# Performance work log

Measured on AMD Instinct MI355X. Metric: run time of the kernel, lower is better.

The kernel has to match this reference:

```python
import jax, jax.numpy as jnp
import numpy as np

B, S, D = 4, 2048, 1024
H = 3 * D  # MLP hidden


def setup_inputs() -> dict:
    key = jax.random.key(0)
    ks = jax.random.split(key, 12)
    s = 1.0 / np.sqrt(D)
    n = lambda k, shape, sc: (jax.random.normal(k, shape, jnp.float32) * sc)
    return {
        "x": n(ks[0], (B, S, D), 1.0),
        "ln1_g": jnp.ones((D,), jnp.float32), "ln1_b": jnp.zeros((D,), jnp.float32),
        "ln2_g": jnp.ones((D,), jnp.float32), "ln2_b": jnp.zeros((D,), jnp.float32),
        "Wq": n(ks[1], (D, D), s), "bq": jnp.zeros((D,), jnp.float32),
        "Wk": n(ks[2], (D, D), s), "bk": jnp.zeros((D,), jnp.float32),
        "Wv": n(ks[3], (D, D), s), "bv": jnp.zeros((D,), jnp.float32),
        "Wi": n(ks[4], (D, 1), s), "bi": jnp.zeros((1,), jnp.float32),
        "Wf": n(ks[5], (D, 1), s), "bf": jnp.zeros((1,), jnp.float32),
        "Wo": n(ks[6], (D, D), s), "bo": jnp.zeros((D,), jnp.float32),
        "W1": n(ks[7], (D, H), s), "b1": jnp.zeros((H,), jnp.float32),
        "W2": n(ks[8], (H, D), 1.0 / np.sqrt(H)), "b2": jnp.zeros((D,), jnp.float32),
    }


def _layernorm(x, g, b, eps=1e-5):
    m = jnp.mean(x, axis=-1, keepdims=True)
    v = jnp.mean(jnp.square(x - m), axis=-1, keepdims=True)
    return (x - m) * jax.lax.rsqrt(v + eps) * g + b


def reference(x, ln1_g, ln1_b, ln2_g, ln2_b, Wq, bq, Wk, bk, Wv, bv,
              Wi, bi, Wf, bf, Wo, bo, W1, b1, W2, b2):
    seq = x.shape[1]
    h = _layernorm(x, ln1_g, ln1_b)
    # q, k computed in the original but unused in the score matrix (kept faithful)
    q = h @ Wq + bq
    k = h @ Wk + bk
    v = h @ Wv + bv                                  # [B,S,D]
    log_f = jax.nn.log_sigmoid(h @ Wf + bf)          # [B,S,1]
    log_i = jax.nn.log_sigmoid(h @ Wi + bi)          # [B,S,1]
    o = jax.nn.sigmoid(h @ Wo + bo)                  # [B,S,D]
    log_f_cum = jnp.cumsum(log_f, axis=1)            # [B,S,1]
    # log_scores[b,t,s] = log_i[b,s] + log_f_cum[b,t] - log_f_cum[b,s]
    log_scores = jnp.swapaxes(log_i, 1, 2) + log_f_cum - jnp.swapaxes(log_f_cum, 1, 2)
    causal = jnp.triu(jnp.full((seq, seq), -1e9, jnp.float32), k=1)
    scores = jnp.exp(log_scores + causal[None])      # [B,S,S]
    scores = scores / (jnp.sum(scores, axis=-1, keepdims=True) + 1e-6)
    attn = scores @ v                                # [B,S,D]
    x = x + o * attn
    h2 = _layernorm(x, ln2_g, ln2_b)
    m = h2 @ W1 + b1
    m = jnp.square(jnp.where(m > 0, m, 0.01 * m))    # LeakyReLU then square
    x = x + m @ W2 + b2
    return x
```

## Files before the change

### kernel.cpp

```cpp
#include <hip/hip_runtime.h>
#include <hip/hip_bf16.h>
#include <cstdint>

#define DI __device__ __forceinline__
typedef unsigned short u16;
using f32x4 = __attribute__((ext_vector_type(4))) float;
using bf16x8 = __attribute__((ext_vector_type(8))) short;

DI float bf16_bits_to_f32(u16 h) { return __uint_as_float(((unsigned int)h) << 16); }
DI u16 f32_to_bf16_bits(float f) {
    unsigned int u = __float_as_uint(f);
    unsigned int lsb = (u >> 16) & 1u;
    u += 0x7fffu + lsb;
    return (u16)(u >> 16);
}
DI float logsigf(float z) {
    if (z >= 0.f) return -log1pf(expf(-z));
    return z - log1pf(expf(z));
}
DI float lsef(float a, float b) {
    float mx = fmaxf(a, b), mn = fminf(a, b);
    return mx + log1pf(expf(mn - mx));
}
DI void ld4(float* d, const float* s) { *(float4*)d = *(const float4*)s; }
DI bool is_bf16(const unsigned int* g1w) { return g1w[0] == 0x3F803F80u; }

struct __align__(8) U4 { u16 a, b, c, d; };
union BF8 { u16 s[8]; uint4 v; };

DI void gload_lds16(const void* gsrc, void* ldst) {
    __builtin_amdgcn_global_load_lds(
        (const __attribute__((address_space(1))) uint32_t*)gsrc,
        (__attribute__((address_space(3))) uint32_t*)ldst,
        16, 0, 0);
}

struct PrepDesc {
    const void* csrc[12];
    unsigned int cdst[12];
    int cn[12];
    const void* tsrc[4];
    unsigned int tdst[4];
    int tR[4], tCd[4];
    int tstart[5];
};
__global__ __launch_bounds__(256) void prep_kernel(
    PrepDesc pd, char* __restrict__ ws, const unsigned int* __restrict__ g1w)
{
    const bool isbf = is_bf16(g1w);
    const int bid = blockIdx.x;
    if (bid < 12) {
        const void* s = pd.csrc[bid];
        float* d = (float*)ws + pd.cdst[bid];
        const int n = pd.cn[bid];
        for (int i = threadIdx.x; i < n; i += 256)
            d[i] = isbf ? bf16_bits_to_f32(((const u16*)s)[i]) : ((const float*)s)[i];
        return;
    }
    __shared__ float tile[64][65];
    const int b2 = bid - 12;
    int e = 0;
    if (b2 >= pd.tstart[1]) e = 1;
    if (b2 >= pd.tstart[2]) e = 2;
    if (b2 >= pd.tstart[3]) e = 3;
    const int local = b2 - pd.tstart[e];
    const int R = pd.tR[e], Cd = pd.tCd[e];
    const int nbx = R >> 6;
    const int r0 = (local % nbx) * 64, c0 = (local / nbx) * 64;
    const void* src = pd.tsrc[e];
    u16* dst = (u16*)ws + pd.tdst[e];
    const int tid = threadIdx.x;
    #pragma unroll
    for (int i = 0; i < 16; ++i) {
        int idx = tid + i * 256;
        int lr = idx >> 6, lc = idx & 63;
        size_t g = (size_t)(r0 + lr) * Cd + c0 + lc;
        tile[lr][lc] = isbf ? bf16_bits_to_f32(((const u16*)src)[g]) : ((const float*)src)[g];
    }
    __syncthreads();
    #pragma unroll
    for (int i = 0; i < 16; ++i) {
        int idx = tid + i * 256;
        int lc2 = idx >> 6, lr2 = idx & 63;
        dst[(size_t)(c0 + lc2) * R + r0 + lr2] = f32_to_bf16_bits(tile[lr2][lc2]);
    }
}

DI float block_reduce_sum256(float v, float* sbuf) {
    #pragma unroll
    for (int off = 32; off > 0; off >>= 1) v += __shfl_down(v, off);
    int lane = threadIdx.x & 63, wid = threadIdx.x >> 6;
    if (lane == 0) sbuf[wid] = v;
    __syncthreads();
    float r = sbuf[0] + sbuf[1] + sbuf[2] + sbuf[3];
    __syncthreads();
    return r;
}

template<bool FI, int MODE>
__global__ __launch_bounds__(256) void ln_kernel(
    const void* __restrict__ Xv, const unsigned int* __restrict__ g1w,
    const float* __restrict__ gam, const float* __restrict__ bet,
    u16* __restrict__ Hout,
    const float* __restrict__ Wi, const float* __restrict__ bi,
    const float* __restrict__ Wf, const float* __restrict__ bf2,
    float* __restrict__ li, float* __restrict__ lf)
{
    __shared__ float sbuf[4];
    int row = blockIdx.x;
    int tid = threadIdx.x;
    size_t base = (size_t)row * 1024 + (size_t)tid * 4;
    float x[4];
    if (MODE == 2 || (MODE == 1 && is_bf16(g1w))) {
        U4 u = *(const U4*)((const u16*)Xv + base);
        x[0] = bf16_bits_to_f32(u.a); x[1] = bf16_bits_to_f32(u.b);
        x[2] = bf16_bits_to_f32(u.c); x[3] = bf16_bits_to_f32(u.d);
    } else {
        ld4(x, (const float*)Xv + base);
    }
    float s = x[0] + x[1] + x[2] + x[3];
    s = block_reduce_sum256(s, sbuf);
    float mean = s * (1.f / 1024.f);
    float d[4], ss = 0.f;
    #pragma unroll
    for (int j = 0; j < 4; ++j) { d[j] = x[j] - mean; ss += d[j] * d[j]; }
    ss = block_reduce_sum256(ss, sbuf);
    float rstd = rsqrtf(ss * (1.f / 1024.f) + 1e-5f);
    float g4[4], b4[4];
    ld4(g4, gam + tid * 4); ld4(b4, bet + tid * 4);
    float h[4];
    #pragma unroll
    for (int j = 0; j < 4; ++j) h[j] = d[j] * rstd * g4[j] + b4[j];
    U4 hu;
    hu.a = f32_to_bf16_bits(h[0]); hu.b = f32_to_bf16_bits(h[1]);
    hu.c = f32_to_bf16_bits(h[2]); hu.d = f32_to_bf16_bits(h[3]);
    *(U4*)(Hout + base) = hu;
    if (FI) {
        float wi4[4], wf4[4];
        ld4(wi4, Wi + tid * 4); ld4(wf4, Wf + tid * 4);
        float pi = 0.f, pf = 0.f;
        #pragma unroll
        for (int j = 0; j < 4; ++j) { pi += h[j] * wi4[j]; pf += h[j] * wf4[j]; }
        pi = block_reduce_sum256(pi, sbuf);
        pf = block_reduce_sum256(pf, sbuf);
        if (tid == 0) {
            li[row] = logsigf(pi + bi[0]);
            lf[row] = logsigf(pf + bf2[0]);
        }
    }
}

__global__ __launch_bounds__(1024) void gates_kernel(
    const float* __restrict__ lf, const float* __restrict__ li,
    float* __restrict__ F, float* __restrict__ rsinv, int S)
{
    __shared__ float p[1024];
    __shared__ float q[1024];
    int b = blockIdx.x, t = threadIdx.x;
    float a = lf[b * S + 2 * t], c = lf[b * S + 2 * t + 1];
    float s2 = a + c;
    p[t] = s2; __syncthreads();
    #pragma unroll
    for (int off = 1; off < 1024; off <<= 1) {
        float add = (t >= off) ? p[t - off] : 0.f;
        __syncthreads();
        p[t] += add;
        __syncthreads();
    }
    float excl = p[t] - s2;
    float F0 = excl + a, F1 = excl + s2;
    F[b * S + 2 * t] = F0; F[b * S + 2 * t + 1] = F1;
    float g0 = li[b * S + 2 * t] - F0;
    float g1 = li[b * S + 2 * t + 1] - F1;
    float m2 = lsef(g0, g1);
    q[t] = m2; __syncthreads();
    #pragma unroll
    for (int off = 1; off < 1024; off <<= 1) {
        float add = (t >= off) ? q[t - off] : -1e30f;
        __syncthreads();
        float nv = lsef(q[t], add);
        __syncthreads();
        q[t] = nv;
        __syncthreads();
    }
    float lprev = (t > 0) ? q[t - 1] : -1e30f;
    float lc0 = lsef(lprev, g0);
    float lc1 = q[t];
    rsinv[b * S + 2 * t]     = 1.f / (expf(F0 + lc0) + 1e-6f);
    rsinv[b * S + 2 * t + 1] = 1.f / (expf(F1 + lc1) + 1e-6f);
}

__global__ __launch_bounds__(256) void wgen_kernel(
    const float* __restrict__ li, const float* __restrict__ F,
    const float* __restrict__ rsinv, u16* __restrict__ Wn)
{
    const int S = 2048;
    const int i = blockIdx.y, b = blockIdx.z;
    const int t0 = i * 128;
    const int s0 = t0 - 128 + (int)blockIdx.x * 64;
    if (s0 < 0) return;
    const int tid = threadIdx.x;
    const int lane = tid & 63, wave = tid >> 6;
    const int colb = (lane & 7) * 8;
    float lv[8], fv[8];
    ld4(lv, li + b * S + s0 + colb); ld4(lv + 4, li + b * S + s0 + colb + 4);
    ld4(fv, F + b * S + s0 + colb);  ld4(fv + 4, F + b * S + s0 + colb + 4);
    float g[8];
    #pragma unroll
    for (int j = 0; j < 8; ++j) g[j] = lv[j] - fv[j];
    #pragma unroll
    for (int r = 0; r < 4; ++r) {
        int row = wave * 32 + r * 8 + (lane >> 3);
        int t = t0 + row;
        float Ft = F[b * S + t];
        float ri = rsinv[b * S + t];
        BF8 wb;
        #pragma unroll
        for (int j = 0; j < 8; ++j) {
            int sg = s0 + colb + j;
            float w = (sg <= t) ? expf(g[j] + Ft) * ri : 0.f;
            wb.s[j] = f32_to_bf16_bits(w);
        }
        *(uint4*)(Wn + ((size_t)b * S + t) * S + s0 + colb) = wb.v;
    }
}

template<int EPI, int TM>
__global__ __launch_bounds__(256) void gemm_bt(
    const u16* __restrict__ A, const u16* __restrict__ Bt,
    const float* __restrict__ bias, u16* __restrict__ C,
    const u16* __restrict__ resid, void* __restrict__ outp,
    const unsigned int* __restrict__ g1w, int M, int N, int K)
{
    constexpr int MFRAG = TM / 32;
    __shared__ short As[TM * 64];
    __shared__ short Bs[128 * 64];
    const int tid = threadIdx.x;
    const int lane = tid & 63;
    const int wave = tid >> 6;
    const int wm = wave >> 1, wn = wave & 1;
    const int m0 = blockIdx.x * TM, n0 = blockIdx.y * 128;

    const int srow = tid >> 3;
    const int sk = ((tid & 7) ^ (srow & 7)) * 8;
    const u16* aB = A  + (size_t)(m0 + srow) * K + sk;
    const u16* bB = Bt + (size_t)(n0 + srow) * K + sk;
    const size_t rowK32 = (size_t)32 * K;
    char* AsB = (char*)As + wave * 1024;
    char* BsB = (char*)Bs + wave * 1024;

    const int hi = lane >> 4;
    const int l7 = lane & 7;
    int ar[MFRAG], br[4];
    #pragma unroll
    for (int f = 0; f < MFRAG; ++f) ar[f] = (wm * (TM / 2) + f * 16 + (lane & 15)) * 64;
    #pragma unroll
    for (int f = 0; f < 4; ++f)     br[f] = (wn * 64 + f * 16 + (lane & 15)) * 64;

    f32x4 acc[MFRAG][4] = {};

    for (int k0 = 0; k0 < K; k0 += 64) {
        const u16* ga = aB; const u16* gb = bB;
        #pragma unroll
        for (int p = 0; p < TM / 32; ++p) { gload_lds16(ga, AsB + p * 4096); ga += rowK32; }
        #pragma unroll
        for (int p = 0; p < 4; ++p) { gload_lds16(gb, BsB + p * 4096); gb += rowK32; }
        aB += 64; bB += 64;
        __syncthreads();
        #pragma unroll
        for (int kk = 0; kk < 2; ++kk) {
            const int co = ((kk * 4 + hi) ^ l7) * 8;
            bf16x8 af[MFRAG], bv[4];
            #pragma unroll
            for (int f = 0; f < MFRAG; ++f) af[f] = *(const bf16x8*)&As[ar[f] + co];
            #pragma unroll
            for (int f = 0; f < 4; ++f) bv[f] = *(const bf16x8*)&Bs[br[f] + co];
            #pragma unroll
            for (int mf = 0; mf < MFRAG; ++mf)
                #pragma unroll
                for (int nf = 0; nf < 4; ++nf)
                    acc[mf][nf] = __builtin_amdgcn_mfma_f32_16x16x32_bf16(
                        af[mf], bv[nf], acc[mf][nf], 0, 0, 0);
        }
        __syncthreads();
    }

    const bool outbf = (EPI == 3) ? is_bf16(g1w) : false;
    #pragma unroll
    for (int mf = 0; mf < MFRAG; ++mf) {
        int r0 = m0 + wm * (TM / 2) + mf * 16 + (lane >> 4) * 4;
        #pragma unroll
        for (int nf = 0; nf < 4; ++nf) {
            int col = n0 + wn * 64 + nf * 16 + (lane & 15);
            float bsc = bias[col];
            #pragma unroll
            for (int j = 0; j < 4; ++j) {
                int row = r0 + j;
                float v = acc[mf][nf][j] + bsc;
                if constexpr (EPI == 2) {
                    float l = v > 0.f ? v : 0.01f * v;
                    C[(size_t)row * N + col] = f32_to_bf16_bits(l * l);
                } else {
                    size_t gi = (size_t)row * N + col;
                    v += bf16_bits_to_f32(resid[gi]);
                    if (outbf) ((u16*)outp)[gi] = f32_to_bf16_bits(v);
                    else       ((float*)outp)[gi] = v;
                }
            }
        }
    }
}

__global__ __launch_bounds__(512, 1) void gemm256(
    const u16* __restrict__ A, const u16* __restrict__ Bt,
    const float* __restrict__ bias, u16* __restrict__ C,
    int M, int N, int K)
{
    __shared__ char lds[131072];
    const int tid = threadIdx.x;
    const int lane = tid & 63, wave = tid >> 6;
    const int wm = wave >> 2, wn = wave & 3;
    const int m0 = blockIdx.x * 256, n0 = blockIdx.y * 256;
    const int nt = K >> 6;

    const int srow8 = lane >> 3;
    const int schk = ((lane & 7) ^ srow8) * 8;
    const u16* sA = A  + (size_t)(m0 + wave * 8 + srow8) * K + schk;
    const u16* sB = Bt + (size_t)(n0 + wave * 8 + srow8) * K + schk;

    auto STAGE = [&](int mat, int half, int buf, int tau) {
        const u16* s = (mat ? sB : sA) + (size_t)(half * 128) * K + tau * 64;
        char* d = lds + buf * 65536 + (mat ? 0 : 32768) + half * 16384 + wave * 1024;
        gload_lds16(s, d);
        gload_lds16(s + (size_t)64 * K, d + 8192);
    };

    const int l15 = lane & 15, hi = lane >> 4, l7 = lane & 7;
    int aro[8], bro[4], co[2];
    #pragma unroll
    for (int f = 0; f < 8; ++f) aro[f] = 32768 + (wm * 128 + f * 16 + l15) * 128;
    #pragma unroll
    for (int f = 0; f < 4; ++f) bro[f] = (wn * 64 + f * 16 + l15) * 128;
    co[0] = ((0 + hi) ^ l7) * 16;
    co[1] = ((4 + hi) ^ l7) * 16;

    f32x4 acc[8][4] = {};

    STAGE(1, 0, 0, 0); STAGE(1, 1, 0, 0); STAGE(0, 0, 0, 0); STAGE(0, 1, 0, 0);
    if (nt > 1) {
        asm volatile("s_waitcnt vmcnt(4)" ::: "memory");
        STAGE(1, 0, 1, 1); STAGE(1, 1, 1, 1); STAGE(0, 0, 1, 1);
        asm volatile("s_waitcnt vmcnt(6)" ::: "memory");
    } else {
        asm volatile("s_waitcnt vmcnt(0)" ::: "memory");
    }
    __builtin_amdgcn_s_barrier();
    __builtin_amdgcn_sched_barrier(0);

    for (int tau = 0; tau < nt; ++tau) {
        const int cur = tau & 1;
        char* bufc = lds + cur * 65536;
        bf16x8 bF[2][4], aF[2][2];

        #pragma unroll
        for (int kk = 0; kk < 2; ++kk) {
            #pragma unroll
            for (int f = 0; f < 4; ++f) bF[kk][f] = *(const bf16x8*)(bufc + bro[f] + co[kk]);
            #pragma unroll
            for (int f = 0; f < 2; ++f) aF[kk][f] = *(const bf16x8*)(bufc + aro[f] + co[kk]);
        }
        if (tau + 1 < nt) STAGE(0, 1, cur ^ 1, tau + 1);
        __builtin_amdgcn_s_barrier();
        asm volatile("s_waitcnt lgkmcnt(0)" ::: "memory");
        __builtin_amdgcn_sched_barrier(0);
        __builtin_amdgcn_s_setprio(1);
        #pragma unroll
        for (int mf = 0; mf < 2; ++mf)
            #pragma unroll
            for (int nf = 0; nf < 4; ++nf)
                #pragma unroll
                for (int kk = 0; kk < 2; ++kk)
                    acc[mf][nf] = __builtin_amdgcn_mfma_f32_16x16x32_bf16(aF[kk][mf], bF[kk][nf], acc[mf][nf], 0, 0, 0);
        __builtin_amdgcn_s_setprio(0);
        __builtin_amdgcn_s_barrier();
        __builtin_amdgcn_sched_barrier(0);

        #pragma unroll
        for (int kk = 0; kk < 2; ++kk)
            #pragma unroll
            for (int f = 0; f < 2; ++f) aF[kk][f] = *(const bf16x8*)(bufc + aro[2 + f] + co[kk]);
        if (tau + 2 < nt) STAGE(1, 0, cur, tau + 2);
        __builtin_amdgcn_s_barrier();
        asm volatile("s_waitcnt lgkmcnt(0)" ::: "memory");
        __builtin_amdgcn_sched_barrier(0);
        __builtin_amdgcn_s_setprio(1);
        #pragma unroll
        for (int mf = 0; mf < 2; ++mf)
            #pragma unroll
            for (int nf = 0; nf < 4; ++nf)
                #pragma unroll
                for (int kk = 0; kk < 2; ++kk)
                    acc[2 + mf][nf] = __builtin_amdgcn_mfma_f32_16x16x32_bf16(aF[kk][mf], bF[kk][nf], acc[2 + mf][nf], 0, 0, 0);
        __builtin_amdgcn_s_setprio(0);
        __builtin_amdgcn_s_barrier();
        __builtin_amdgcn_sched_barrier(0);

        #pragma unroll
        for (int kk = 0; kk < 2; ++kk)
            #pragma unroll
            for (int f = 0; f < 2; ++f) aF[kk][f] = *(const bf16x8*)(bufc + aro[4 + f] + co[kk]);
        if (tau + 2 < nt) STAGE(1, 1, cur, tau + 2);
        __builtin_amdgcn_s_barrier();
        asm volatile("s_waitcnt lgkmcnt(0)" ::: "memory");
        __builtin_amdgcn_sched_barrier(0);
        __builtin_amdgcn_s_setprio(1);
        #pragma unroll
        for (int mf = 0; mf < 2; ++mf)
            #pragma unroll
            for (int nf = 0; nf < 4; ++nf)
                #pragma unroll
                for (int kk = 0; kk < 2; ++kk)
                    acc[4 + mf][nf] = __builtin_amdgcn_mfma_f32_16x16x32_bf16(aF[kk][mf], bF[kk][nf], acc[4 + mf][nf], 0, 0, 0);
        __builtin_amdgcn_s_setprio(0);
        __builtin_amdgcn_s_barrier();
        __builtin_amdgcn_sched_barrier(0);

        #pragma unroll
        for (int kk = 0; kk < 2; ++kk)
            #pragma unroll
            for (int f = 0; f < 2; ++f) aF[kk][f] = *(const bf16x8*)(bufc + aro[6 + f] + co[kk]);
        if (tau + 2 < nt) STAGE(0, 0, cur, tau + 2);
        if (tau + 2 < nt) asm volatile("s_waitcnt vmcnt(6)" ::: "memory");
        else              asm volatile("s_waitcnt vmcnt(0)" ::: "memory");
        __builtin_amdgcn_s_barrier();
        asm volatile("s_waitcnt lgkmcnt(0)" ::: "memory");
        __builtin_amdgcn_sched_barrier(0);
        __builtin_amdgcn_s_setprio(1);
        #pragma unroll
        for (int mf = 0; mf < 2; ++mf)
            #pragma unroll
            for (int nf = 0; nf < 4; ++nf)
                #pragma unroll
                for (int kk = 0; kk < 2; ++kk)
                    acc[6 + mf][nf] = __builtin_amdgcn_mfma_f32_16x16x32_bf16(aF[kk][mf], bF[kk][nf], acc[6 + mf][nf], 0, 0, 0);
        __builtin_amdgcn_s_setprio(0);
        __builtin_amdgcn_s_barrier();
        __builtin_amdgcn_sched_barrier(0);
    }

    #pragma unroll
    for (int mf = 0; mf < 8; ++mf) {
        int rb = m0 + wm * 128 + mf * 16 + hi * 4;
        #pragma unroll
        for (int nf = 0; nf < 4; ++nf) {
            int col = n0 + wn * 64 + nf * 16 + l15;
            float bsc = bias[col];
            #pragma unroll
            for (int j = 0; j < 4; ++j) {
                int row = rb + j;
                float v = acc[mf][nf][j] + bsc;
                float l = v > 0.f ? v : 0.01f * v;
                C[(size_t)row * N + col] = f32_to_bf16_bits(l * l);
            }
        }
    }
}

__global__ __launch_bounds__(256) void gemm_vo(
    const u16* __restrict__ H, const u16* __restrict__ WOT, const u16* __restrict__ WVT,
    const float* __restrict__ bo, const float* __restrict__ bv,
    u16* __restrict__ O, u16* __restrict__ V)
{
    __shared__ short As[64 * 64];
    __shared__ short Bs[128 * 64];
    const int tid = threadIdx.x;
    const int lane = tid & 63;
    const int wave = tid >> 6;
    const int wm = wave >> 1, wn = wave & 1;
    const int K = 1024;

    const int z = blockIdx.z;
    const u16* A;  const u16* Bt; int m0, n0, N;
    u16* C;
    if (z == 0) {
        A = H;   Bt = WOT; m0 = blockIdx.x * 64; n0 = blockIdx.y * 128; N = 1024; C = O;
    } else {
        const int flat = blockIdx.x * 8 + blockIdx.y;
        A = WVT; Bt = H;   m0 = (flat & 15) * 64; n0 = (flat >> 4) * 128; N = 8192; C = V;
    }

    const int srow = tid >> 3;
    const int sk = ((tid & 7) ^ (srow & 7)) * 8;
    const u16* aB = A  + (size_t)(m0 + srow) * K + sk;
    const u16* bB = Bt + (size_t)(n0 + srow) * K + sk;
    const size_t rowK32 = (size_t)32 * K;
    char* AsB = (char*)As + wave * 1024;
    char* BsB = (char*)Bs + wave * 1024;

    const int hi = lane >> 4;
    const int l7 = lane & 7;
    int ar[2], br[4];
    #pragma unroll
    for (int f = 0; f < 2; ++f) ar[f] = (wm * 32 + f * 16 + (lane & 15)) * 64;
    #pragma unroll
    for (int f = 0; f < 4; ++f) br[f] = (wn * 64 + f * 16 + (lane & 15)) * 64;

    f32x4 acc[2][4] = {};

    for (int k0 = 0; k0 < K; k0 += 64) {
        const u16* ga = aB; const u16* gb = bB;
        #pragma unroll
        for (int p = 0; p < 2; ++p) { gload_lds16(ga, AsB + p * 4096); ga += rowK32; }
        #pragma unroll
        for (int p = 0; p < 4; ++p) { gload_lds16(gb, BsB + p * 4096); gb += rowK32; }
        aB += 64; bB += 64;
        __syncthreads();
        #pragma unroll
        for (int kk = 0; kk < 2; ++kk) {
            const int co = ((kk * 4 + hi) ^ l7) * 8;
            bf16x8 af[2], bv4[4];
            #pragma unroll
            for (int f = 0; f < 2; ++f) af[f] = *(const bf16x8*)&As[ar[f] + co];
            #pragma unroll
            for (int f = 0; f < 4; ++f) bv4[f] = *(const bf16x8*)&Bs[br[f] + co];
            #pragma unroll
            for (int mf = 0; mf < 2; ++mf)
                #pragma unroll
                for (int nf = 0; nf < 4; ++nf)
                    acc[mf][nf] = __builtin_amdgcn_mfma_f32_16x16x32_bf16(
                        af[mf], bv4[nf], acc[mf][nf], 0, 0, 0);
        }
        __syncthreads();
    }

    #pragma unroll
    for (int mf = 0; mf < 2; ++mf) {
        int r0 = m0 + wm * 32 + mf * 16 + (lane >> 4) * 4;
        #pragma unroll
        for (int nf = 0; nf < 4; ++nf) {
            int col = n0 + wn * 64 + nf * 16 + (lane & 15);
            #pragma unroll
            for (int j = 0; j < 4; ++j) {
                int row = r0 + j;
                float v;
                if (z == 0) {
                    v = acc[mf][nf][j] + bo[col];
                    v = 1.f / (1.f + expf(-v));
                } else {
                    v = acc[mf][nf][j] + bv[row];
                }
                C[(size_t)row * N + col] = f32_to_bf16_bits(v);
            }
        }
    }
}

__global__ __launch_bounds__(256) void attn_gemm(
    const u16* __restrict__ Wn, const u16* __restrict__ Vt,
    const u16* __restrict__ Ob, const void* __restrict__ Xraw,
    const unsigned int* __restrict__ g1w, u16* __restrict__ XF)
{
    const int S = 2048, D = 1024, NT = 8192;
    __shared__ short As[128 * 64];
    __shared__ short Bs[128 * 64];
    const int b  = blockIdx.z;
    const int it = blockIdx.x;
    const int t0 = it * 128;
    const int d0 = blockIdx.y * 128;
    const int tid = threadIdx.x;
    const int lane = tid & 63;
    const int wave = tid >> 6;
    const int wm = wave >> 1, wn = wave & 1;

    const int srow = tid >> 3;
    const int sk = ((tid & 7) ^ (srow & 7)) * 8;
    const u16* aB = Wn + ((size_t)b * S + t0 + srow) * S + sk;
    const u16* bB = Vt + (size_t)(d0 + srow) * NT + b * S + sk;
    char* AsB = (char*)As + wave * 1024;
    char* BsB = (char*)Bs + wave * 1024;

    const int hi = lane >> 4;
    const int l7 = lane & 7;
    int ar[4], br[4];
    #pragma unroll
    for (int f = 0; f < 4; ++f) {
        ar[f] = (wm * 64 + f * 16 + (lane & 15)) * 64;
        br[f] = (wn * 64 + f * 16 + (lane & 15)) * 64;
    }

    f32x4 acc[4][4] = {};
    const int first = (2 * it - 2 > 0) ? (2 * it - 2) : 0;
    const int nst = (2 * it + 1) - first + 1;
    for (int st = 0; st < nst; ++st) {
        const int s0 = (first + st) * 64;
        const u16* ga = aB + s0; const u16* gb = bB + s0;
        #pragma unroll
        for (int p = 0; p < 4; ++p) { gload_lds16(ga, AsB + p * 4096); ga += (size_t)32 * S; }
        #pragma unroll
        for (int p = 0; p < 4; ++p) { gload_lds16(gb, BsB + p * 4096); gb += (size_t)32 * NT; }
        __syncthreads();
        #pragma unroll
        for (int kk = 0; kk < 2; ++kk) {
            const int co = ((kk * 4 + hi) ^ l7) * 8;
            bf16x8 af[4], bv[4];
            #pragma unroll
            for (int f = 0; f < 4; ++f) af[f] = *(const bf16x8*)&As[ar[f] + co];
            #pragma unroll
            for (int f = 0; f < 4; ++f) bv[f] = *(const bf16x8*)&Bs[br[f] + co];
            #pragma unroll
            for (int mf = 0; mf < 4; ++mf)
                #pragma unroll
                for (int nf = 0; nf < 4; ++nf)
                    acc[mf][nf] = __builtin_amdgcn_mfma_f32_16x16x32_bf16(
                        af[mf], bv[nf], acc[mf][nf], 0, 0, 0);
        }
        __syncthreads();
    }

    const bool isbf = is_bf16(g1w);
    #pragma unroll
    for (int mf = 0; mf < 4; ++mf) {
        #pragma unroll
        for (int j = 0; j < 4; ++j) {
            int r = wm * 64 + mf * 16 + (lane >> 4) * 4 + j;
            int t = t0 + r;
            #pragma unroll
            for (int nf = 0; nf < 4; ++nf) {
                int dcol = d0 + wn * 64 + nf * 16 + (lane & 15);
                size_t base = ((size_t)b * S + t) * D + dcol;
                float o = bf16_bits_to_f32(Ob[base]);
                float xv = isbf ? bf16_bits_to_f32(((const u16*)Xraw)[base])
                                : ((const float*)Xraw)[base];
                XF[base] = f32_to_bf16_bits(xv + o * acc[mf][nf][j]);
            }
        }
    }
}

static constexpr size_t OFB_LI   = 4096;
static constexpr size_t OFB_LF   = 36864;
static constexpr size_t OFB_F    = 69632;
static constexpr size_t OFB_G1   = 102400;
static constexpr size_t OFB_B1LN = 106496;
static constexpr size_t OFB_G2   = 110592;
static constexpr size_t OFB_B2LN = 114688;
static constexpr size_t OFB_BV   = 118784;
static constexpr size_t OFB_BO   = 122880;
static constexpr size_t OFB_WI   = 126976;
static constexpr size_t OFB_WF   = 131072;
static constexpr size_t OFB_B1   = 135168;
static constexpr size_t OFB_B2B  = 147456;
static constexpr size_t OFB_BI   = 151552;
static constexpr size_t OFB_BF   = 152576;
static constexpr size_t OFB_RS   = 200704;
static constexpr size_t OFB_XF   = 1048576;
static constexpr size_t OFB_H    = OFB_XF + 33554432;
static constexpr size_t OFB_V    = OFB_H + 16777216;
static constexpr size_t OFB_O    = OFB_V + 16777216;
static constexpr size_t OFB_M    = OFB_O + 16777216;
static constexpr size_t OFB_WVT  = OFB_M + 50331648;
static constexpr size_t OFB_WOT  = OFB_WVT + 2097152;
static constexpr size_t OFB_W1T  = OFB_WOT + 2097152;
static constexpr size_t OFB_W2T  = OFB_W1T + 6291456;
static constexpr size_t WS_BYTES = OFB_W2T + 6291456;

extern "C" void kernel_launch(void* const* d_in, const int* in_sizes, int n_in,
                              void* d_out, int out_size, void* d_ws, size_t ws_size,
                              hipStream_t stream) {
    (void)in_sizes; (void)n_in; (void)out_size;
    if (ws_size < WS_BYTES) return;
    char* ws = (char*)d_ws;
    const unsigned int* g1w = (const unsigned int*)d_in[1];
    auto FP = [&](size_t off) { return (float*)(ws + off); };
    auto HP = [&](size_t off) { return (u16*)(ws + off); };

    PrepDesc pd;
    const int   srcIdx[12] = {1, 2, 3, 4, 10, 16, 11, 12, 13, 14, 18, 20};
    const size_t dstOff[12] = {OFB_G1, OFB_B1LN, OFB_G2, OFB_B2LN, OFB_BV, OFB_BO,
                               OFB_WI, OFB_BI, OFB_WF, OFB_BF, OFB_B1, OFB_B2B};
    const int   cnt[12] = {1024, 1024, 1024, 1024, 1024, 1024, 1024, 1, 1024, 1, 3072, 1024};
    for (int e = 0; e < 12; ++e) {
        pd.csrc[e] = d_in[srcIdx[e]];
        pd.cdst[e] = (unsigned int)(dstOff[e] / 4);
        pd.cn[e] = cnt[e];
    }
    pd.tsrc[0] = d_in[9];  pd.tdst[0] = (unsigned int)(OFB_WVT / 2); pd.tR[0] = 1024; pd.tCd[0] = 1024;
    pd.tsrc[1] = d_in[15]; pd.tdst[1] = (unsigned int)(OFB_WOT / 2); pd.tR[1] = 1024; pd.tCd[1] = 1024;
    pd.tsrc[2] = d_in[17]; pd.tdst[2] = (unsigned int)(OFB_W1T / 2); pd.tR[2] = 1024; pd.tCd[2] = 3072;
    pd.tsrc[3] = d_in[19]; pd.tdst[3] = (unsigned int)(OFB_W2T / 2); pd.tR[3] = 3072; pd.tCd[3] = 1024;
    pd.tstart[0] = 0; pd.tstart[1] = 256; pd.tstart[2] = 512; pd.tstart[3] = 1280; pd.tstart[4] = 2048;
    prep_kernel<<<2060, 256, 0, stream>>>(pd, ws, g1w);

    ln_kernel<true, 1><<<8192, 256, 0, stream>>>(
        d_in[0], g1w, FP(OFB_G1), FP(OFB_B1LN), HP(OFB_H),
        FP(OFB_WI), FP(OFB_BI), FP(OFB_WF), FP(OFB_BF),
        FP(OFB_LI), FP(OFB_LF));

    gates_kernel<<<4, 1024, 0, stream>>>(FP(OFB_LF), FP(OFB_LI), FP(OFB_F), FP(OFB_RS), 2048);

    wgen_kernel<<<dim3(4, 16, 4), 256, 0, stream>>>(
        FP(OFB_LI), FP(OFB_F), FP(OFB_RS), HP(OFB_M));

    gemm_vo<<<dim3(128, 8, 2), 256, 0, stream>>>(
        HP(OFB_H), HP(OFB_WOT), HP(OFB_WVT), FP(OFB_BO), FP(OFB_BV),
        HP(OFB_O), HP(OFB_V));

    attn_gemm<<<dim3(16, 8, 4), 256, 0, stream>>>(
        HP(OFB_M), HP(OFB_V), HP(OFB_O), d_in[0], g1w, HP(OFB_XF));

    ln_kernel<false, 2><<<8192, 256, 0, stream>>>(
        HP(OFB_XF), g1w, FP(OFB_G2), FP(OFB_B2LN), HP(OFB_H),
        nullptr, nullptr, nullptr, nullptr, nullptr, nullptr);

    gemm256<<<dim3(32, 12), 512, 0, stream>>>(
        HP(OFB_H), HP(OFB_W1T), FP(OFB_B1), HP(OFB_M), 8192, 3072, 1024);
    gemm_bt<3, 64><<<dim3(128, 8), 256, 0, stream>>>(
        HP(OFB_M), HP(OFB_W2T), FP(OFB_B2B), nullptr, HP(OFB_XF),
        d_out, g1w, 8192, 1024, 3072);
}
```

Before: 267.8 us.

## Double-buffer LDS tiles in gemm_bt and gemm_vo to prefetch the next K tile

```diff
diff --git a/kernel.cpp b/kernel.cpp
--- a/kernel.cpp
+++ b/kernel.cpp
@@ -233,8 +233,8 @@
     const unsigned int* __restrict__ g1w, int M, int N, int K)
 {
     constexpr int MFRAG = TM / 32;
-    __shared__ short As[TM * 64];
-    __shared__ short Bs[128 * 64];
+    __shared__ short As[2][TM * 64];
+    __shared__ short Bs[2][128 * 64];
     const int tid = threadIdx.x;
     const int lane = tid & 63;
     const int wave = tid >> 6;
@@ -243,11 +243,20 @@
 
     const int srow = tid >> 3;
     const int sk = ((tid & 7) ^ (srow & 7)) * 8;
-    const u16* aB = A  + (size_t)(m0 + srow) * K + sk;
-    const u16* bB = Bt + (size_t)(n0 + srow) * K + sk;
+    const u16* aBase = A  + (size_t)(m0 + srow) * K + sk;
+    const u16* bBase = Bt + (size_t)(n0 + srow) * K + sk;
     const size_t rowK32 = (size_t)32 * K;
-    char* AsB = (char*)As + wave * 1024;
-    char* BsB = (char*)Bs + wave * 1024;
+
+    auto STAGE = [&](int buf, int t) {
+        const u16* ga = aBase + t * 64;
+        const u16* gb = bBase + t * 64;
+        char* AsB = (char*)&As[buf][0] + wave * 1024;
+        char* BsB = (char*)&Bs[buf][0] + wave * 1024;
+        #pragma unroll
+        for (int p = 0; p < TM / 32; ++p) { gload_lds16(ga, AsB + p * 4096); ga += rowK32; }
+        #pragma unroll
+        for (int p = 0; p < 4; ++p) { gload_lds16(gb, BsB + p * 4096); gb += rowK32; }
+    };
 
     const int hi = lane >> 4;
     const int l7 = lane & 7;
@@ -258,23 +267,24 @@
     for (int f = 0; f < 4; ++f)     br[f] = (wn * 64 + f * 16 + (lane & 15)) * 64;
 
     f32x4 acc[MFRAG][4] = {};
-
-    for (int k0 = 0; k0 < K; k0 += 64) {
-        const u16* ga = aB; const u16* gb = bB;
-        #pragma unroll
-        for (int p = 0; p < TM / 32; ++p) { gload_lds16(ga, AsB + p * 4096); ga += rowK32; }
-        #pragma unroll
-        for (int p = 0; p < 4; ++p) { gload_lds16(gb, BsB + p * 4096); gb += rowK32; }
-        aB += 64; bB += 64;
-        __syncthreads();
+    const int nt = K >> 6;
+
+    STAGE(0, 0);
+    __syncthreads();
+
+    for (int t = 0; t < nt; ++t) {
+        const int cur = t & 1;
+        if (t + 1 < nt) STAGE(cur ^ 1, t + 1);
+        const short* Ab = &As[cur][0];
+        const short* Bb = &Bs[cur][0];
         #pragma unroll
         for (int kk = 0; kk < 2; ++kk) {
             const int co = ((kk * 4 + hi) ^ l7) * 8;
             bf16x8 af[MFRAG], bv[4];
             #pragma unroll
-            for (int f = 0; f < MFRAG; ++f) af[f] = *(const bf16x8*)&As[ar[f] + co];
-            #pragma unroll
-            for (int f = 0; f < 4; ++f) bv[f] = *(const bf16x8*)&Bs[br[f] + co];
+            for (int f = 0; f < MFRAG; ++f) af[f] = *(const bf16x8*)&Ab[ar[f] + co];
+            #pragma unroll
+            for (int f = 0; f < 4; ++f) bv[f] = *(const bf16x8*)&Bb[br[f] + co];
             #pragma unroll
             for (int mf = 0; mf < MFRAG; ++mf)
                 #pragma unroll
@@ -471,8 +481,8 @@
     const float* __restrict__ bo, const float* __restrict__ bv,
     u16* __restrict__ O, u16* __restrict__ V)
 {
-    __shared__ short As[64 * 64];
-    __shared__ short Bs[128 * 64];
+    __shared__ short As[2][64 * 64];
+    __shared__ short Bs[2][128 * 64];
     const int tid = threadIdx.x;
     const int lane = tid & 63;
     const int wave = tid >> 6;
@@ -491,11 +501,20 @@
 
     const int srow = tid >> 3;
     const int sk = ((tid & 7) ^ (srow & 7)) * 8;
-    const u16* aB = A  + (size_t)(m0 + srow) * K + sk;
-    const u16* bB = Bt + (size_t)(n0 + srow) * K + sk;
+    const u16* aBase = A  + (size_t)(m0 + srow) * K + sk;
+    const u16* bBase = Bt + (size_t)(n0 + srow) * K + sk;
     const size_t rowK32 = (size_t)32 * K;
-    char* AsB = (char*)As + wave * 1024;
-    char* BsB = (char*)Bs + wave * 1024;
+
+    auto STAGE = [&](int buf, int t) {
+        const u16* ga = aBase + t * 64;
+        const u16* gb = bBase + t * 64;
+        char* AsB = (char*)&As[buf][0] + wave * 1024;
+        char* BsB = (char*)&Bs[buf][0] + wave * 1024;
+        #pragma unroll
+        for (int p = 0; p < 2; ++p) { gload_lds16(ga, AsB + p * 4096); ga += rowK32; }
+        #pragma unroll
+        for (int p = 0; p < 4; ++p) { gload_lds16(gb, BsB + p * 4096); gb += rowK32; }
+    };
 
     const int hi = lane >> 4;
     const int l7 = lane & 7;
@@ -506,23 +525,24 @@
     for (int f = 0; f < 4; ++f) br[f] = (wn * 64 + f * 16 + (lane & 15)) * 64;
 
     f32x4 acc[2][4] = {};
-
-    for (int k0 = 0; k0 < K; k0 += 64) {
-        const u16* ga = aB; const u16* gb = bB;
-        #pragma unroll
-        for (int p = 0; p < 2; ++p) { gload_lds16(ga, AsB + p * 4096); ga += rowK32; }
-        #pragma unroll
-        for (int p = 0; p < 4; ++p) { gload_lds16(gb, BsB + p * 4096); gb += rowK32; }
-        aB += 64; bB += 64;
-        __syncthreads();
+    const int nt = K >> 6;
+
+    STAGE(0, 0);
+    __syncthreads();
+
+    for (int t = 0; t < nt; ++t) {
+        const int cur = t & 1;
+        if (t + 1 < nt) STAGE(cur ^ 1, t + 1);
+        const short* Ab = &As[cur][0];
+        const short* Bb = &Bs[cur][0];
         #pragma unroll
         for (int kk = 0; kk < 2; ++kk) {
             const int co = ((kk * 4 + hi) ^ l7) * 8;
             bf16x8 af[2], bv4[4];
             #pragma unroll
-            for (int f = 0; f < 2; ++f) af[f] = *(const bf16x8*)&As[ar[f] + co];
-            #pragma unroll
-            for (int f = 0; f < 4; ++f) bv4[f] = *(const bf16x8*)&Bs[br[f] + co];
+            for (int f = 0; f < 2; ++f) af[f] = *(const bf16x8*)&Ab[ar[f] + co];
+            #pragma unroll
+            for (int f = 0; f < 4; ++f) bv4[f] = *(const bf16x8*)&Bb[br[f] + co];
             #pragma unroll
             for (int mf = 0; mf < 2; ++mf)
                 #pragma unroll
```

Result: slower. 305.6 us (+14.1%).
